# Optimization experiments

Hardware: AMD Instinct MI355X
Metric: run time of the kernel (lower is better)

## Reference

```python
import jax, jax.numpy as jnp
import numpy as np

B, N, C, H = 8, 1024, 768, 12
D = C // H
SCALE = D ** -0.5


def setup_inputs() -> dict:
    key = jax.random.key(0)
    k1, k2, k3 = jax.random.split(key, 3)
    x = jax.random.normal(k1, (B, N, C), dtype=jnp.float32)
    w_qkv = jax.random.normal(k2, (C, 3 * C), dtype=jnp.float32) * (C ** -0.5)
    w_proj = jax.random.normal(k3, (C, C), dtype=jnp.float32) * (C ** -0.5)
    b_proj = jnp.zeros((C,), dtype=jnp.float32)
    return {"x": x, "w_qkv": w_qkv, "w_proj": w_proj, "b_proj": b_proj}


def reference(x, w_qkv, w_proj, b_proj):
    Bx, Nx, Cx = x.shape
    # qkv projection (no bias), split into q,k,v with shape [B, H, N, D]
    qkv = (x @ w_qkv).reshape(Bx, Nx, 3, H, D).transpose(2, 0, 3, 1, 4)
    q, k, v = qkv[0], qkv[1], qkv[2]
    # full attention matrix [B, H, N, N] (matches torch module's explicit materialization)
    attn = jnp.einsum('bhqd,bhkd->bhqk', q, k) * SCALE
    attn = jax.nn.softmax(attn, axis=-1)
    out = jnp.einsum('bhqk,bhkd->bhqd', attn, v)
    out = out.transpose(0, 2, 1, 3).reshape(Bx, Nx, Cx)
    return out @ w_proj + b_proj
```

## Files before the change

kernel.cpp:

```cpp
#include <hip/hip_runtime.h>


typedef unsigned short u16;
typedef short s16x8 __attribute__((ext_vector_type(8)));
typedef float f32x4 __attribute__((ext_vector_type(4)));
typedef u16   u16x8 __attribute__((ext_vector_type(8)));
typedef u16   u16x4 __attribute__((ext_vector_type(4)));

__device__ __forceinline__ u16 f2bf(float f) {
    unsigned int u = __builtin_bit_cast(unsigned int, f);
    u += 0x7FFFu + ((u >> 16) & 1u);
    return (u16)(u >> 16);
}

__device__ __forceinline__ void gload16(const u16* g, u16* l) {
    __builtin_amdgcn_global_load_lds(
        (const __attribute__((address_space(1))) unsigned int*)g,
        (__attribute__((address_space(3))) unsigned int*)l, 16, 0, 0);
}

__global__ __launch_bounds__(256) void prep(
    const float* __restrict__ x, u16* __restrict__ xb,
    const float* __restrict__ wq, u16* __restrict__ wqT,
    const float* __restrict__ wp, u16* __restrict__ wpT) {
    __shared__ float ts[32][33];
    const int g = blockIdx.x, tid = threadIdx.x;
    if (g < 3072) {
        const size_t i = ((size_t)g * 256 + tid) * 8;
        float4 v0 = *(const float4*)(x + i);
        float4 v1 = *(const float4*)(x + i + 4);
        u16x8 p;
        p[0] = f2bf(v0.x); p[1] = f2bf(v0.y); p[2] = f2bf(v0.z); p[3] = f2bf(v0.w);
        p[4] = f2bf(v1.x); p[5] = f2bf(v1.y); p[6] = f2bf(v1.z); p[7] = f2bf(v1.w);
        *(u16x8*)(xb + i) = p;
        return;
    }
    const float* in; u16* out; int K, Nc, n0, k0;
    if (g < 4800) {
        int gg = g - 3072; in = wq; out = wqT; K = 768; Nc = 2304;
        n0 = (gg % 72) * 32; k0 = (gg / 72) * 32;
    } else {
        int gg = g - 4800; in = wp; out = wpT; K = 768; Nc = 768;
        n0 = (gg % 24) * 32; k0 = (gg / 24) * 32;
    }
    const int tx = tid & 31, ty = tid >> 5;
#pragma unroll
    for (int j = 0; j < 4; ++j) {
        int r = ty + j * 8;
        ts[r][tx] = in[(size_t)(k0 + r) * Nc + n0 + tx];
    }
    __syncthreads();
#pragma unroll
    for (int j = 0; j < 4; ++j) {
        int r = ty + j * 8;
        out[(size_t)(n0 + r) * K + k0 + tx] = f2bf(ts[tx][r]);
    }
}

template<bool SWAP>
__device__ __forceinline__ void gemm_loop_128(
    f32x4 (&acc)[4][4], const u16* __restrict__ A, const u16* __restrict__ B,
    u16* As, u16* Bs, int m0, int n0, int lane, int w) {
    const int m15 = lane & 15, quad = lane >> 4;
    const int wy = w >> 1, wx = w & 1;
    const int qsw8 = (quad ^ ((m15 >> 1) & 3)) * 8;
    const int srow16 = lane >> 2;
    const int scg = ((lane & 3) ^ ((lane >> 3) & 3)) * 8;
    const size_t gA = (size_t)(m0 + w * 32 + srow16) * 768 + scg;
    const size_t gB = (size_t)(n0 + w * 32 + srow16) * 768 + scg;

    auto stage = [&](int buf, int s) {
        const int k0 = (s < 24 ? s : 0) * 32;
        u16* da = As + buf * 4096 + (w * 32) * 32;
        u16* db = Bs + buf * 4096 + (w * 32) * 32;
        gload16(A + gA + k0,            da);
        gload16(A + gA + 16 * 768 + k0, da + 16 * 32);
        gload16(B + gB + k0,            db);
        gload16(B + gB + 16 * 768 + k0, db + 16 * 32);
    };

    stage(0, 0);
    const int arow = (wy * 64 + m15) * 32 + qsw8;
    const int brow = (wx * 64 + m15) * 32 + qsw8;

#pragma unroll 2
    for (int s = 0; s < 24; ++s) {
        const int cur = s & 1;
        stage(cur ^ 1, s + 1);
        asm volatile("s_waitcnt vmcnt(4)" ::: "memory");
        __builtin_amdgcn_s_barrier();
        const u16* Ap = As + cur * 4096;
        const u16* Bp = Bs + cur * 4096;
        s16x8 av[4], bv[4];
#pragma unroll
        for (int ri = 0; ri < 4; ++ri)
            av[ri] = *(const s16x8*)(Ap + arow + ri * 512);
#pragma unroll
        for (int ci = 0; ci < 4; ++ci)
            bv[ci] = *(const s16x8*)(Bp + brow + ci * 512);
        __builtin_amdgcn_s_setprio(1);
#pragma unroll
        for (int ri = 0; ri < 4; ++ri)
#pragma unroll
            for (int ci = 0; ci < 4; ++ci) {
                if (SWAP)
                    acc[ri][ci] = __builtin_amdgcn_mfma_f32_16x16x32_bf16(bv[ci], av[ri], acc[ri][ci], 0, 0, 0);
                else
                    acc[ri][ci] = __builtin_amdgcn_mfma_f32_16x16x32_bf16(av[ri], bv[ci], acc[ri][ci], 0, 0, 0);
            }
        __builtin_amdgcn_s_setprio(0);
        __builtin_amdgcn_s_barrier();
    }
}

__global__ __launch_bounds__(256, 4) void gemm_qkv(
    const u16* __restrict__ Aq, const u16* __restrict__ Bt,
    u16* __restrict__ qb, u16* __restrict__ kb, u16* __restrict__ vbT) {
    __shared__ __align__(16) u16 As[2 * 128 * 32];
    __shared__ __align__(16) u16 Bs[2 * 128 * 32];
    const int tid = threadIdx.x;
    const int lane = tid & 63, w = tid >> 6;
    const int m15 = lane & 15, quad = lane >> 4;
    const int wy = w >> 1, wx = w & 1;
    const int g = blockIdx.x;
    const int xcd = g & 7, s = g >> 3;
    const int yt = xcd * 8 + (s & 7), xt = s >> 3;
    const int m0 = yt * 128, n0 = xt * 128;
    const int which = xt / 6;

    f32x4 acc[4][4] = {};
    if (which < 2)
        gemm_loop_128<true >(acc, Aq, Bt, As, Bs, m0, n0, lane, w);
    else
        gemm_loop_128<false>(acc, Aq, Bt, As, Bs, m0, n0, lane, w);

    const int b   = m0 >> 10;
    const int r0  = (m0 & 1023) + wy * 64;
    const int n0p = n0 - which * 768;
    const int h   = (n0p >> 6) + wx;
    const size_t bhi = (size_t)(b * 12 + h);
    if (which == 2) {
#pragma unroll
        for (int ri = 0; ri < 4; ++ri)
#pragma unroll
            for (int ci = 0; ci < 4; ++ci) {
                u16x4 pk;
#pragma unroll
                for (int rg = 0; rg < 4; ++rg) pk[rg] = f2bf(acc[ri][ci][rg]);
                const int d   = ci * 16 + m15;
                const int tok = r0 + ri * 16 + (quad << 2);
                *(u16x4*)&vbT[(bhi * 64 + d) * 1024 + tok] = pk;
            }
    } else {
        u16* dst = which ? kb : qb;
#pragma unroll
        for (int ri = 0; ri < 4; ++ri)
#pragma unroll
            for (int ci = 0; ci < 4; ++ci) {
                u16x4 pk;
#pragma unroll
                for (int rg = 0; rg < 4; ++rg) pk[rg] = f2bf(acc[ri][ci][rg]);
                const int tok = r0 + ri * 16 + m15;
                const int d   = ci * 16 + (quad << 2);
                *(u16x4*)&dst[(bhi * 1024 + tok) * 64 + d] = pk;
            }
    }
}

__global__ __launch_bounds__(256, 4) void gemm_proj(
    const u16* __restrict__ A, const u16* __restrict__ Bt,
    const float* __restrict__ bias, float* __restrict__ out) {
    __shared__ __align__(16) u16 As[2 * 128 * 32];
    __shared__ __align__(16) u16 Bs[2 * 128 * 32];
    const int tid = threadIdx.x;
    const int lane = tid & 63, w = tid >> 6;
    const int m15 = lane & 15, quad = lane >> 4;
    const int wy = w >> 1, wx = w & 1;
    const int g = blockIdx.x;
    const int xcd = g & 7, s = g >> 3;
    const int yt = xcd * 8 + (s & 7), xt = s >> 3;
    const int m0 = yt * 128, n0 = xt * 128;

    f32x4 acc[4][4] = {};
    gemm_loop_128<false>(acc, A, Bt, As, Bs, m0, n0, lane, w);

#pragma unroll
    for (int ri = 0; ri < 4; ++ri) {
        int mb = m0 + wy * 64 + ri * 16 + (quad << 2);
#pragma unroll
        for (int ci = 0; ci < 4; ++ci) {
            int n = n0 + wx * 64 + ci * 16 + m15;
            float bv_ = bias[n];
#pragma unroll
            for (int rg = 0; rg < 4; ++rg)
                out[(size_t)(mb + rg) * 768 + n] = acc[ri][ci][rg] + bv_;
        }
    }
}

#define KS 72

__global__ __launch_bounds__(256) void attn_mfma(
    const u16* __restrict__ qb, const u16* __restrict__ kb,
    const u16* __restrict__ vbT, u16* __restrict__ aout) {
    __shared__ __align__(16) u16 Ks[64 * KS];
    __shared__ __align__(16) u16 Vs[64 * KS];
    __shared__ __align__(16) u16 Ps[8][16 * KS];
    const int tid = threadIdx.x, lane = tid & 63, w = tid >> 6;
    const int m15 = lane & 15, quad = lane >> 4;
    const int g = blockIdx.x;
    const int xcd = g & 7, s = g >> 3;
    const int bh = xcd * 12 + (s % 12);
    const int q0 = (s / 12) * 128;

    s16x8 aq[2][2];
#pragma unroll
    for (int qs = 0; qs < 2; ++qs) {
        const u16* qp = qb + ((size_t)bh * 1024 + q0 + w * 32 + qs * 16 + m15) * 64 + quad * 8;
        aq[qs][0] = *(const s16x8*)qp;
        aq[qs][1] = *(const s16x8*)(qp + 32);
    }

    s16x8 bones;
#pragma unroll
    for (int j = 0; j < 8; ++j) bones[j] = (m15 == 0) ? (short)0x3F80 : (short)0;

    f32x4 oacc[2][4] = {};
    f32x4 lacc[2] = {};

    const int srow = tid >> 2;
    const int soff = (tid & 3) * 16;
    const u16* kbase = kb + (size_t)bh * 1024 * 64;
    const u16* vbase = vbT + (size_t)bh * 64 * 1024;
    const float CE   = 0.125f * 1.44269504f;
    const float MOFF = 12.0f * 1.44269504f;

    for (int kt = 0; kt < 16; ++kt) {
        __syncthreads();
        const u16* kpp = kbase + ((size_t)kt * 64 + srow) * 64 + soff;
        const u16* vpp = vbase + (size_t)srow * 1024 + kt * 64 + soff;
        *(u16x8*)&Ks[srow * KS + soff]     = *(const u16x8*)kpp;
        *(u16x8*)&Ks[srow * KS + soff + 8] = *(const u16x8*)(kpp + 8);
        *(u16x8*)&Vs[srow * KS + soff]     = *(const u16x8*)vpp;
        *(u16x8*)&Vs[srow * KS + soff + 8] = *(const u16x8*)(vpp + 8);
        __syncthreads();

        f32x4 sacc[2][4] = {};
#pragma unroll
        for (int t = 0; t < 4; ++t)
#pragma unroll
            for (int ch = 0; ch < 2; ++ch) {
                s16x8 ak = *(const s16x8*)&Ks[(t * 16 + m15) * KS + quad * 8 + 32 * ch];
                sacc[0][t] = __builtin_amdgcn_mfma_f32_16x16x32_bf16(ak, aq[0][ch], sacc[0][t], 0, 0, 0);
                sacc[1][t] = __builtin_amdgcn_mfma_f32_16x16x32_bf16(ak, aq[1][ch], sacc[1][t], 0, 0, 0);
            }

#pragma unroll
        for (int qs = 0; qs < 2; ++qs)
#pragma unroll
            for (int t = 0; t < 4; ++t) {
                u16x4 pk;
#pragma unroll
                for (int reg = 0; reg < 4; ++reg) {
                    float pv = __builtin_amdgcn_exp2f(sacc[qs][t][reg] * CE - MOFF);
                    unsigned int u = __builtin_bit_cast(unsigned int, pv);
                    pk[reg] = (u16)(u >> 16);
                }
                *(u16x4*)&Ps[w * 2 + qs][m15 * KS + t * 16 + quad * 4] = pk;
            }

        s16x8 ap[2][2];
#pragma unroll
        for (int qs = 0; qs < 2; ++qs) {
            ap[qs][0] = *(const s16x8*)&Ps[w * 2 + qs][m15 * KS + quad * 8];
            ap[qs][1] = *(const s16x8*)&Ps[w * 2 + qs][m15 * KS + quad * 8 + 32];
#pragma unroll
            for (int ch = 0; ch < 2; ++ch)
                lacc[qs] = __builtin_amdgcn_mfma_f32_16x16x32_bf16(ap[qs][ch], bones, lacc[qs], 0, 0, 0);
        }
#pragma unroll
        for (int di = 0; di < 4; ++di)
#pragma unroll
            for (int ch = 0; ch < 2; ++ch) {
                s16x8 bv = *(const s16x8*)&Vs[(di * 16 + m15) * KS + quad * 8 + 32 * ch];
                oacc[0][di] = __builtin_amdgcn_mfma_f32_16x16x32_bf16(ap[0][ch], bv, oacc[0][di], 0, 0, 0);
                oacc[1][di] = __builtin_amdgcn_mfma_f32_16x16x32_bf16(ap[1][ch], bv, oacc[1][di], 0, 0, 0);
            }
    }

    const int b = bh / 12, h = bh - b * 12;
#pragma unroll
    for (int qs = 0; qs < 2; ++qs) {
        float linv[4];
#pragma unroll
        for (int reg = 0; reg < 4; ++reg)
            linv[reg] = 1.0f / __shfl(lacc[qs][reg], lane & 48);
#pragma unroll
        for (int di = 0; di < 4; ++di)
#pragma unroll
            for (int reg = 0; reg < 4; ++reg) {
                int q = q0 + w * 32 + qs * 16 + quad * 4 + reg;
                aout[((size_t)b * 1024 + q) * 768 + h * 64 + di * 16 + m15] =
                    f2bf(oacc[qs][di][reg] * linv[reg]);
            }
    }
}

extern "C" void kernel_launch(void* const* d_in, const int* in_sizes, int n_in,
                              void* d_out, int out_size, void* d_ws, size_t ws_size,
                              hipStream_t stream) {
    const float* x      = (const float*)d_in[0];
    const float* w_qkv  = (const float*)d_in[1];
    const float* w_proj = (const float*)d_in[2];
    const float* b_proj = (const float*)d_in[3];
    float* out = (float*)d_out;

    char* ws = (char*)d_ws;
    u16* wqkvT  = (u16*)ws;  ws += (size_t)2304 * 768 * 2;
    u16* wprojT = (u16*)ws;  ws += (size_t)768 * 768 * 2;
    u16* qb     = (u16*)ws;  ws += (size_t)96 * 1024 * 64 * 2;
    u16* kb     = (u16*)ws;  ws += (size_t)96 * 1024 * 64 * 2;
    u16* vbT    = (u16*)ws;  ws += (size_t)96 * 1024 * 64 * 2;
    u16* aout   = (u16*)ws;  ws += (size_t)8192 * 768 * 2;
    u16* xb     = aout;

    prep<<<dim3(5376), 256, 0, stream>>>(x, xb, w_qkv, wqkvT, w_proj, wprojT);
    gemm_qkv<<<dim3(1152), 256, 0, stream>>>(xb, wqkvT, qb, kb, vbT);
    attn_mfma<<<dim3(768), 256, 0, stream>>>(qb, kb, vbT, aout);
    gemm_proj<<<dim3(384), 256, 0, stream>>>(aout, wprojT, b_proj, out);
}
```

Baseline: 190.1 us.

## Replace LDS-staged GEMM tiles with direct global-to-register double-buffered loads

Both GEMMs (QKV and output projection) now drop the shared-memory staging through global_load_lds and barriers. Each wave loads its MFMA operand fragments straight from global memory (L2) into registers, with a two-deep register double buffer across K steps. This removes LDS traffic and the per-iteration barriers, and the launch bounds hint of 4 blocks per SM is dropped. In exchange, each wave re-fetches data from L2 that neighbouring waves share (no intra-block reuse), the per-lane loads are strided rows, and register pressure rises.

```diff
diff --git a/kernel.cpp b/kernel.cpp
--- a/kernel.cpp
+++ b/kernel.cpp
@@ -11,12 +11,6 @@
     unsigned int u = __builtin_bit_cast(unsigned int, f);
     u += 0x7FFFu + ((u >> 16) & 1u);
     return (u16)(u >> 16);
-}
-
-__device__ __forceinline__ void gload16(const u16* g, u16* l) {
-    __builtin_amdgcn_global_load_lds(
-        (const __attribute__((address_space(1))) unsigned int*)g,
-        (__attribute__((address_space(3))) unsigned int*)l, 16, 0, 0);
 }
 
 __global__ __launch_bounds__(256) void prep(
@@ -58,66 +52,63 @@
 }
 
 template<bool SWAP>
-__device__ __forceinline__ void gemm_loop_128(
+__device__ __forceinline__ void mfma16(f32x4 (&acc)[4][4],
+                                       const s16x8 (&av)[4], const s16x8 (&bv)[4]) {
+#pragma unroll
+    for (int ri = 0; ri < 4; ++ri)
+#pragma unroll
+        for (int ci = 0; ci < 4; ++ci) {
+            if (SWAP)
+                acc[ri][ci] = __builtin_amdgcn_mfma_f32_16x16x32_bf16(bv[ci], av[ri], acc[ri][ci], 0, 0, 0);
+            else
+                acc[ri][ci] = __builtin_amdgcn_mfma_f32_16x16x32_bf16(av[ri], bv[ci], acc[ri][ci], 0, 0, 0);
+        }
+}
+
+template<bool SWAP>
+__device__ __forceinline__ void gemm_l2_loop(
     f32x4 (&acc)[4][4], const u16* __restrict__ A, const u16* __restrict__ B,
-    u16* As, u16* Bs, int m0, int n0, int lane, int w) {
+    int m0, int n0, int lane, int w) {
     const int m15 = lane & 15, quad = lane >> 4;
     const int wy = w >> 1, wx = w & 1;
-    const int qsw8 = (quad ^ ((m15 >> 1) & 3)) * 8;
-    const int srow16 = lane >> 2;
-    const int scg = ((lane & 3) ^ ((lane >> 3) & 3)) * 8;
-    const size_t gA = (size_t)(m0 + w * 32 + srow16) * 768 + scg;
-    const size_t gB = (size_t)(n0 + w * 32 + srow16) * 768 + scg;
-
-    auto stage = [&](int buf, int s) {
-        const int k0 = (s < 24 ? s : 0) * 32;
-        u16* da = As + buf * 4096 + (w * 32) * 32;
-        u16* db = Bs + buf * 4096 + (w * 32) * 32;
-        gload16(A + gA + k0,            da);
-        gload16(A + gA + 16 * 768 + k0, da + 16 * 32);
-        gload16(B + gB + k0,            db);
-        gload16(B + gB + 16 * 768 + k0, db + 16 * 32);
-    };
-
-    stage(0, 0);
-    const int arow = (wy * 64 + m15) * 32 + qsw8;
-    const int brow = (wx * 64 + m15) * 32 + qsw8;
-
-#pragma unroll 2
-    for (int s = 0; s < 24; ++s) {
-        const int cur = s & 1;
-        stage(cur ^ 1, s + 1);
-        asm volatile("s_waitcnt vmcnt(4)" ::: "memory");
-        __builtin_amdgcn_s_barrier();
-        const u16* Ap = As + cur * 4096;
-        const u16* Bp = Bs + cur * 4096;
-        s16x8 av[4], bv[4];
-#pragma unroll
-        for (int ri = 0; ri < 4; ++ri)
-            av[ri] = *(const s16x8*)(Ap + arow + ri * 512);
-#pragma unroll
-        for (int ci = 0; ci < 4; ++ci)
-            bv[ci] = *(const s16x8*)(Bp + brow + ci * 512);
-        __builtin_amdgcn_s_setprio(1);
-#pragma unroll
-        for (int ri = 0; ri < 4; ++ri)
-#pragma unroll
-            for (int ci = 0; ci < 4; ++ci) {
-                if (SWAP)
-                    acc[ri][ci] = __builtin_amdgcn_mfma_f32_16x16x32_bf16(bv[ci], av[ri], acc[ri][ci], 0, 0, 0);
-                else
-                    acc[ri][ci] = __builtin_amdgcn_mfma_f32_16x16x32_bf16(av[ri], bv[ci], acc[ri][ci], 0, 0, 0);
-            }
-        __builtin_amdgcn_s_setprio(0);
-        __builtin_amdgcn_s_barrier();
-    }
-}
-
-__global__ __launch_bounds__(256, 4) void gemm_qkv(
+    const u16* ap[4];
+    const u16* bp[4];
+#pragma unroll
+    for (int ri = 0; ri < 4; ++ri)
+        ap[ri] = A + (size_t)(m0 + wy * 64 + ri * 16 + m15) * 768 + quad * 8;
+#pragma unroll
+    for (int ci = 0; ci < 4; ++ci)
+        bp[ci] = B + (size_t)(n0 + wx * 64 + ci * 16 + m15) * 768 + quad * 8;
+
+    s16x8 a0[4], b0[4], a1[4], b1[4];
+#pragma unroll
+    for (int i = 0; i < 4; ++i) {
+        a0[i] = *(const s16x8*)ap[i];
+        b0[i] = *(const s16x8*)bp[i];
+    }
+
+#pragma unroll
+    for (int s = 0; s < 24; s += 2) {
+#pragma unroll
+        for (int i = 0; i < 4; ++i) {
+            a1[i] = *(const s16x8*)(ap[i] + (s + 1) * 32);
+            b1[i] = *(const s16x8*)(bp[i] + (s + 1) * 32);
+        }
+        mfma16<SWAP>(acc, a0, b0);
+        if (s + 2 < 24) {
+#pragma unroll
+            for (int i = 0; i < 4; ++i) {
+                a0[i] = *(const s16x8*)(ap[i] + (s + 2) * 32);
+                b0[i] = *(const s16x8*)(bp[i] + (s + 2) * 32);
+            }
+        }
+        mfma16<SWAP>(acc, a1, b1);
+    }
+}
+
+__global__ __launch_bounds__(256) void gemm_qkv(
     const u16* __restrict__ Aq, const u16* __restrict__ Bt,
     u16* __restrict__ qb, u16* __restrict__ kb, u16* __restrict__ vbT) {
-    __shared__ __align__(16) u16 As[2 * 128 * 32];
-    __shared__ __align__(16) u16 Bs[2 * 128 * 32];
     const int tid = threadIdx.x;
     const int lane = tid & 63, w = tid >> 6;
     const int m15 = lane & 15, quad = lane >> 4;
@@ -130,9 +121,9 @@
 
     f32x4 acc[4][4] = {};
     if (which < 2)
-        gemm_loop_128<true >(acc, Aq, Bt, As, Bs, m0, n0, lane, w);
+        gemm_l2_loop<true >(acc, Aq, Bt, m0, n0, lane, w);
     else
-        gemm_loop_128<false>(acc, Aq, Bt, As, Bs, m0, n0, lane, w);
+        gemm_l2_loop<false>(acc, Aq, Bt, m0, n0, lane, w);
 
     const int b   = m0 >> 10;
     const int r0  = (m0 & 1023) + wy * 64;
@@ -167,11 +158,9 @@
     }
 }
 
-__global__ __launch_bounds__(256, 4) void gemm_proj(
+__global__ __launch_bounds__(256) void gemm_proj(
     const u16* __restrict__ A, const u16* __restrict__ Bt,
     const float* __restrict__ bias, float* __restrict__ out) {
-    __shared__ __align__(16) u16 As[2 * 128 * 32];
-    __shared__ __align__(16) u16 Bs[2 * 128 * 32];
     const int tid = threadIdx.x;
     const int lane = tid & 63, w = tid >> 6;
     const int m15 = lane & 15, quad = lane >> 4;
@@ -182,7 +171,7 @@
     const int m0 = yt * 128, n0 = xt * 128;
 
     f32x4 acc[4][4] = {};
-    gemm_loop_128<false>(acc, A, Bt, As, Bs, m0, n0, lane, w);
+    gemm_l2_loop<false>(acc, A, Bt, m0, n0, lane, w);
 
 #pragma unroll
     for (int ri = 0; ri < 4; ++ri) {
```

Result: slower. 284.9 us (+49.9%).
